# Kernel optimization log

Measured on AMD Instinct MI355X. Metric: run time of the kernel, lower is better.

The kernel has to match this reference:

```python
import math
import jax, jax.numpy as jnp
import numpy as np

B, L, S, H, E, D = 4, 2048, 2048, 8, 64, 64

def setup_inputs() -> dict:
    key = jax.random.key(0)
    kq, kk, kv = jax.random.split(key, 3)
    return {
        "queries": jax.random.normal(kq, (B, L, H, E), dtype=jnp.float32),
        "keys": jax.random.normal(kk, (B, S, H, E), dtype=jnp.float32),
        "values": jax.random.normal(kv, (B, S, H, D), dtype=jnp.float32),
    }

def reference(queries, keys, values):
    E_ = queries.shape[-1]
    scale = 1.0 / math.sqrt(E_)
    # scores: [B, H, L, S]
    scores = jnp.einsum('blhe,bshe->bhls', queries, keys)
    A = jax.nn.softmax(scale * scores, axis=-1)
    # dropout omitted (eval mode / p=0.0)
    out = jnp.einsum('bhls,bshd->blhd', A, values)
    return out
```

## Files before the change

kernel.cpp:

```cpp
#include <hip/hip_runtime.h>
#include <hip/hip_bf16.h>


#define BNUM 4
#define LLEN 2048
#define SLEN 2048
#define HNUM 8
#define EDIM 64

typedef __attribute__((ext_vector_type(8))) short s16x8;
typedef __attribute__((ext_vector_type(8))) _Float16 hf16x8;
typedef __attribute__((ext_vector_type(2))) __fp16 fp16x2;
typedef __attribute__((ext_vector_type(4))) float f32x4;

__device__ __forceinline__ short f2h(float f) {
    union { _Float16 h; short s; } u;
    u.h = (_Float16)f;
    return u.s;
}

__device__ __forceinline__ s16x8 pk8(float4 a, float4 b) {
    union { fp16x2 h[4]; s16x8 v; } u;
    u.h[0] = __builtin_amdgcn_cvt_pkrtz(a.x, a.y);
    u.h[1] = __builtin_amdgcn_cvt_pkrtz(a.z, a.w);
    u.h[2] = __builtin_amdgcn_cvt_pkrtz(b.x, b.y);
    u.h[3] = __builtin_amdgcn_cvt_pkrtz(b.z, b.w);
    return u.v;
}

#if __has_builtin(__builtin_amdgcn_global_load_lds)
#define HAVE_GLL 1
#else
#define HAVE_GLL 0
#endif

__device__ __forceinline__ void stage16(const short* g, short* l) {
#if HAVE_GLL
    __builtin_amdgcn_global_load_lds(
        (const __attribute__((address_space(1))) void*)g,
        (__attribute__((address_space(3))) void*)l, 16, 0, 0);
#else
    *(s16x8*)l = *(const s16x8*)g;
#endif
}

__global__ __launch_bounds__(256)
void prep(const float* __restrict__ Kg, const float* __restrict__ Vg,
          short* __restrict__ Kc, short* __restrict__ Vt)
{
    __shared__ short tile[EDIM][80];
    if (blockIdx.y == 0) {
        const int t = blockIdx.x * 256 + threadIdx.x;
        const int e8 = t & 7;
        const int tmp = t >> 3;
        const int h = tmp & 7;
        const int tmp2 = tmp >> 3;
        const int s = tmp2 & (SLEN - 1);
        const int b = tmp2 >> 11;
        const float4* src = (const float4*)(Kg + (((size_t)(b * SLEN + s) * HNUM + h) * EDIM + e8 * 8));
        float4 a = src[0], bb = src[1];
        *(s16x8*)(Kc + ((size_t)((b * HNUM + h) * SLEN + s) * EDIM + e8 * 8)) = pk8(a, bb);
    } else {
        if (blockIdx.x >= 1024) return;
        const int x = blockIdx.x;
        const int s0 = (x & 31) * 64;
        const int bh = x >> 5;
        const int b = bh >> 3, h = bh & 7;
        {
            const int sr = threadIdx.x >> 2, dc = (threadIdx.x & 3) * 16;
            const float4* src = (const float4*)(Vg + (((size_t)(b * SLEN + s0 + sr) * HNUM + h) * EDIM + dc));
            #pragma unroll
            for (int j4 = 0; j4 < 4; ++j4) {
                float4 a = src[j4];
                tile[dc + j4*4 + 0][sr] = f2h(a.x);
                tile[dc + j4*4 + 1][sr] = f2h(a.y);
                tile[dc + j4*4 + 2][sr] = f2h(a.z);
                tile[dc + j4*4 + 3][sr] = f2h(a.w);
            }
        }
        __syncthreads();
        {
            const int dr = threadIdx.x >> 2, sc = (threadIdx.x & 3) * 16;
            short* dst = Vt + ((size_t)((b * HNUM + h) * EDIM + dr) * SLEN + s0 + sc);
            *(s16x8*)dst       = *(const s16x8*)&tile[dr][sc];
            *(s16x8*)(dst + 8) = *(const s16x8*)&tile[dr][sc + 8];
        }
    }
}

__global__ __launch_bounds__(128, 2)
void fa_fwd(const float* __restrict__ Qg, const short* __restrict__ Kc,
            const short* __restrict__ Vt, float* __restrict__ Og)
{
    __shared__ short sKV[8704];
    __shared__ float sL[2][64];

    const int tid  = threadIdx.x;
    const int wave = tid >> 6;
    const int lane = tid & 63;
    const int m    = lane & 15;
    const int quad = lane >> 4;

    const int lin  = (int)blockIdx.x;
    const int logi = ((lin & 7) << 7) + (lin >> 3);
    const int qx = logi & 31;
    const int h  = (logi >> 5) & 7;
    const int b  = logi >> 8;
    const int qbase = qx * 64;
    const int bh = b * HNUM + h;

    const short* Kbh = Kc + (size_t)bh * SLEN * EDIM;
    const short* Vbh = Vt + (size_t)bh * EDIM * SLEN;

    const int l3 = lane >> 3;
    const int ksrcE = (wave * 32 + l3) * EDIM + ((lane & 7) ^ (l3 & 3)) * 8;
    const int ksrcO = (wave * 32 + l3) * EDIM + ((lane & 7) ^ (4 + (l3 & 3))) * 8;
    const int vsrcB = (lane >> 2) * SLEN + wave * 32 + ((lane & 3) ^ ((lane >> 2) & 3)) * 8;
    short* kdstB = sKV + (wave * 256 + lane) * 8;
    short* vdstB = sKV + 4096 + (wave * 256 + lane) * 8;

#define STAGE_TILE(s0)                                                        \
    do {                                                                      \
        _Pragma("unroll")                                                     \
        for (int p = 0; p < 4; ++p) {                                         \
            const int ks = ((p & 1) ? ksrcO : ksrcE) + (p >> 1) * 1024 + (p & 1) * 512; \
            stage16(Kbh + (size_t)(s0) * EDIM + ks, kdstB + p * 512);         \
            stage16(Vbh + (s0) + vsrcB + p * 16 * SLEN, vdstB + p * 512);     \
        }                                                                     \
    } while (0)

    const float csc = 0.18033688011112042f;
    hf16x8 qfrag[4][2];
    #pragma unroll
    for (int qt = 0; qt < 4; ++qt)
        #pragma unroll
        for (int kb = 0; kb < 2; ++kb) {
            const float* qp = Qg + ((size_t)(b * LLEN + qbase + qt * 16 + m) * HNUM + h) * EDIM
                              + kb * 32 + quad * 8;
            float4 x0 = *(const float4*)qp;
            float4 x1 = *(const float4*)(qp + 4);
            float4 y0 = {x0.x*csc, x0.y*csc, x0.z*csc, x0.w*csc};
            float4 y1 = {x1.x*csc, x1.y*csc, x1.z*csc, x1.w*csc};
            union { s16x8 s; hf16x8 h; } u;
            u.s = pk8(y0, y1);
            qfrag[qt][kb] = u.h;
        }

    const int gk  = ((m >> 2) & 1) * 4 + (m & 3);
    const int pi0 = 8 * (m >> 2) + (m & 3);
    const int kOff00 = (wave * 32 + pi0)     * 64 + ((quad)     ^ gk) * 8;
    const int kOff01 = (wave * 32 + pi0)     * 64 + ((4 + quad) ^ gk) * 8;
    const int kOff10 = (wave * 32 + pi0 + 4) * 64 + ((quad)     ^ gk) * 8;
    const int kOff11 = (wave * 32 + pi0 + 4) * 64 + ((4 + quad) ^ gk) * 8;
    const int vOffB  = 4096 + wave * 2048 + m * 32 + ((quad ^ (m & 3)) * 8);

    hf16x8 vones;
    #pragma unroll
    for (int j = 0; j < 8; ++j) vones[j] = (_Float16)1.0f;

    f32x4 oacc[4][4];
    f32x4 lacc[4];
    #pragma unroll
    for (int i = 0; i < 4; ++i) {
        #pragma unroll
        for (int j = 0; j < 4; ++j) oacc[i][j] = (f32x4){0.f, 0.f, 0.f, 0.f};
        lacc[i] = (f32x4){0.f, 0.f, 0.f, 0.f};
    }

    STAGE_TILE(0);
    __syncthreads();

    for (int s0 = 0; s0 < SLEN; s0 += 64) {
        hf16x8 kf00 = *(const hf16x8*)(sKV + kOff00);
        hf16x8 kf01 = *(const hf16x8*)(sKV + kOff01);
        hf16x8 kf10 = *(const hf16x8*)(sKV + kOff10);
        hf16x8 kf11 = *(const hf16x8*)(sKV + kOff11);
        hf16x8 vf0 = *(const hf16x8*)(sKV + vOffB);
        hf16x8 vf1 = *(const hf16x8*)(sKV + vOffB + 512);
        hf16x8 vf2 = *(const hf16x8*)(sKV + vOffB + 1024);
        hf16x8 vf3 = *(const hf16x8*)(sKV + vOffB + 1536);

        __syncthreads();

        if (s0 + 64 < SLEN) STAGE_TILE(s0 + 64);

        #pragma unroll
        for (int qt = 0; qt < 4; ++qt) {
            f32x4 a0 = {0.f, 0.f, 0.f, 0.f};
            f32x4 a1 = {0.f, 0.f, 0.f, 0.f};
            a0 = __builtin_amdgcn_mfma_f32_16x16x32_f16(kf00, qfrag[qt][0], a0, 0, 0, 0);
            a0 = __builtin_amdgcn_mfma_f32_16x16x32_f16(kf01, qfrag[qt][1], a0, 0, 0, 0);
            a1 = __builtin_amdgcn_mfma_f32_16x16x32_f16(kf10, qfrag[qt][0], a1, 0, 0, 0);
            a1 = __builtin_amdgcn_mfma_f32_16x16x32_f16(kf11, qfrag[qt][1], a1, 0, 0, 0);
            float p0 = __builtin_amdgcn_exp2f(a0[0]);
            float p1 = __builtin_amdgcn_exp2f(a0[1]);
            float p2 = __builtin_amdgcn_exp2f(a0[2]);
            float p3 = __builtin_amdgcn_exp2f(a0[3]);
            float p4 = __builtin_amdgcn_exp2f(a1[0]);
            float p5 = __builtin_amdgcn_exp2f(a1[1]);
            float p6 = __builtin_amdgcn_exp2f(a1[2]);
            float p7 = __builtin_amdgcn_exp2f(a1[3]);
            union { fp16x2 h2[4]; hf16x8 v; } pu;
            pu.h2[0] = __builtin_amdgcn_cvt_pkrtz(p0, p1);
            pu.h2[1] = __builtin_amdgcn_cvt_pkrtz(p2, p3);
            pu.h2[2] = __builtin_amdgcn_cvt_pkrtz(p4, p5);
            pu.h2[3] = __builtin_amdgcn_cvt_pkrtz(p6, p7);
            hf16x8 pf = pu.v;
            lacc[qt] = __builtin_amdgcn_mfma_f32_16x16x32_f16(pf, vones, lacc[qt], 0, 0, 0);
            oacc[qt][0] = __builtin_amdgcn_mfma_f32_16x16x32_f16(pf, vf0, oacc[qt][0], 0, 0, 0);
            oacc[qt][1] = __builtin_amdgcn_mfma_f32_16x16x32_f16(pf, vf1, oacc[qt][1], 0, 0, 0);
            oacc[qt][2] = __builtin_amdgcn_mfma_f32_16x16x32_f16(pf, vf2, oacc[qt][2], 0, 0, 0);
            oacc[qt][3] = __builtin_amdgcn_mfma_f32_16x16x32_f16(pf, vf3, oacc[qt][3], 0, 0, 0);
        }

        __syncthreads();
    }

    if (m == 0) {
        #pragma unroll
        for (int qt = 0; qt < 4; ++qt)
            #pragma unroll
            for (int r = 0; r < 4; ++r)
                sL[wave][qt * 16 + quad * 4 + r] = lacc[qt][r];
    }
    __syncthreads();

    float* sO = (float*)sKV;
    if (wave == 0) {
        #pragma unroll
        for (int qt = 0; qt < 4; ++qt)
            #pragma unroll
            for (int dt = 0; dt < 4; ++dt)
                #pragma unroll
                for (int r = 0; r < 4; ++r)
                    sO[(qt * 16 + quad * 4 + r) * 68 + dt * 16 + m] = oacc[qt][dt][r];
    }
    __syncthreads();
    if (wave == 1) {
        #pragma unroll
        for (int qt = 0; qt < 4; ++qt)
            #pragma unroll
            for (int dt = 0; dt < 4; ++dt)
                #pragma unroll
                for (int r = 0; r < 4; ++r)
                    sO[(qt * 16 + quad * 4 + r) * 68 + dt * 16 + m] += oacc[qt][dt][r];
    }
    __syncthreads();

    {
        const int q = tid >> 1;
        const int dcol = (tid & 1) * 32;
        const float l = sL[0][q] + sL[1][q];
        const float inv = 1.0f / l;
        float* orow = Og + ((size_t)(b * LLEN + qbase + q) * HNUM + h) * EDIM + dcol;
        #pragma unroll
        for (int j = 0; j < 8; ++j) {
            float4 v = *(const float4*)(sO + q * 68 + dcol + j * 4);
            v.x *= inv; v.y *= inv; v.z *= inv; v.w *= inv;
            *(float4*)(orow + j * 4) = v;
        }
    }
}

extern "C" void kernel_launch(void* const* d_in, const int* in_sizes, int n_in,
                              void* d_out, int out_size, void* d_ws, size_t ws_size,
                              hipStream_t stream) {
    const float* Q = (const float*)d_in[0];
    const float* K = (const float*)d_in[1];
    const float* V = (const float*)d_in[2];
    float* O = (float*)d_out;

    const size_t NE = (size_t)BNUM * LLEN * HNUM * EDIM;
    short* Kc = (short*)d_ws;
    short* Vt = Kc + NE;

    prep<<<dim3(2048, 2), dim3(256), 0, stream>>>(K, V, Kc, Vt);
    fa_fwd<<<dim3(1024), dim3(128), 0, stream>>>(Q, Kc, Vt, O);
}
```

Measured before the change: 137.2 us.

## Split keys across four waves per block with 32-query tiles

Reworks the attention kernel to use 256-thread blocks of four waves. Each block now owns 32 queries instead of 64, and each wave processes a 32-key slice of a 128-key staged tile. The grid doubles to 2048 blocks and the per-wave accumulators shrink, so more waves can be resident and the memory latency is spread more finely. In exchange, each block reuses the staged K/V data for half as many queries, and the final cross-wave reduction becomes a serial four-step shared-memory accumulate with a barrier after each step.

```diff
diff --git a/kernel.cpp b/kernel.cpp
--- a/kernel.cpp
+++ b/kernel.cpp
@@ -88,12 +88,12 @@
     }
 }
 
-__global__ __launch_bounds__(128, 2)
+__global__ __launch_bounds__(256, 4)
 void fa_fwd(const float* __restrict__ Qg, const short* __restrict__ Kc,
             const short* __restrict__ Vt, float* __restrict__ Og)
 {
-    __shared__ short sKV[8704];
-    __shared__ float sL[2][64];
+    __shared__ short sKV[16384];
+    __shared__ float sL[4][32];
 
     const int tid  = threadIdx.x;
     const int wave = tid >> 6;
@@ -102,11 +102,11 @@
     const int quad = lane >> 4;
 
     const int lin  = (int)blockIdx.x;
-    const int logi = ((lin & 7) << 7) + (lin >> 3);
-    const int qx = logi & 31;
-    const int h  = (logi >> 5) & 7;
-    const int b  = logi >> 8;
-    const int qbase = qx * 64;
+    const int logi = ((lin & 7) << 8) + (lin >> 3);
+    const int qx = logi & 63;
+    const int h  = (logi >> 6) & 7;
+    const int b  = logi >> 9;
+    const int qbase = qx * 32;
     const int bh = b * HNUM + h;
 
     const short* Kbh = Kc + (size_t)bh * SLEN * EDIM;
@@ -117,7 +117,7 @@
     const int ksrcO = (wave * 32 + l3) * EDIM + ((lane & 7) ^ (4 + (l3 & 3))) * 8;
     const int vsrcB = (lane >> 2) * SLEN + wave * 32 + ((lane & 3) ^ ((lane >> 2) & 3)) * 8;
     short* kdstB = sKV + (wave * 256 + lane) * 8;
-    short* vdstB = sKV + 4096 + (wave * 256 + lane) * 8;
+    short* vdstB = sKV + 8192 + (wave * 256 + lane) * 8;
 
 #define STAGE_TILE(s0)                                                        \
     do {                                                                      \
@@ -130,9 +130,9 @@
     } while (0)
 
     const float csc = 0.18033688011112042f;
-    hf16x8 qfrag[4][2];
-    #pragma unroll
-    for (int qt = 0; qt < 4; ++qt)
+    hf16x8 qfrag[2][2];
+    #pragma unroll
+    for (int qt = 0; qt < 2; ++qt)
         #pragma unroll
         for (int kb = 0; kb < 2; ++kb) {
             const float* qp = Qg + ((size_t)(b * LLEN + qbase + qt * 16 + m) * HNUM + h) * EDIM
@@ -152,16 +152,16 @@
     const int kOff01 = (wave * 32 + pi0)     * 64 + ((4 + quad) ^ gk) * 8;
     const int kOff10 = (wave * 32 + pi0 + 4) * 64 + ((quad)     ^ gk) * 8;
     const int kOff11 = (wave * 32 + pi0 + 4) * 64 + ((4 + quad) ^ gk) * 8;
-    const int vOffB  = 4096 + wave * 2048 + m * 32 + ((quad ^ (m & 3)) * 8);
+    const int vOffB  = 8192 + wave * 2048 + m * 32 + ((quad ^ (m & 3)) * 8);
 
     hf16x8 vones;
     #pragma unroll
     for (int j = 0; j < 8; ++j) vones[j] = (_Float16)1.0f;
 
-    f32x4 oacc[4][4];
-    f32x4 lacc[4];
-    #pragma unroll
-    for (int i = 0; i < 4; ++i) {
+    f32x4 oacc[2][4];
+    f32x4 lacc[2];
+    #pragma unroll
+    for (int i = 0; i < 2; ++i) {
         #pragma unroll
         for (int j = 0; j < 4; ++j) oacc[i][j] = (f32x4){0.f, 0.f, 0.f, 0.f};
         lacc[i] = (f32x4){0.f, 0.f, 0.f, 0.f};
@@ -170,7 +170,7 @@
     STAGE_TILE(0);
     __syncthreads();
 
-    for (int s0 = 0; s0 < SLEN; s0 += 64) {
+    for (int s0 = 0; s0 < SLEN; s0 += 128) {
         hf16x8 kf00 = *(const hf16x8*)(sKV + kOff00);
         hf16x8 kf01 = *(const hf16x8*)(sKV + kOff01);
         hf16x8 kf10 = *(const hf16x8*)(sKV + kOff10);
@@ -182,10 +182,10 @@
 
         __syncthreads();
 
-        if (s0 + 64 < SLEN) STAGE_TILE(s0 + 64);
-
-        #pragma unroll
-        for (int qt = 0; qt < 4; ++qt) {
+        if (s0 + 128 < SLEN) STAGE_TILE(s0 + 128);
+
+        #pragma unroll
+        for (int qt = 0; qt < 2; ++qt) {
             f32x4 a0 = {0.f, 0.f, 0.f, 0.f};
             f32x4 a1 = {0.f, 0.f, 0.f, 0.f};
             a0 = __builtin_amdgcn_mfma_f32_16x16x32_f16(kf00, qfrag[qt][0], a0, 0, 0, 0);
@@ -218,7 +218,7 @@
 
     if (m == 0) {
         #pragma unroll
-        for (int qt = 0; qt < 4; ++qt)
+        for (int qt = 0; qt < 2; ++qt)
             #pragma unroll
             for (int r = 0; r < 4; ++r)
                 sL[wave][qt * 16 + quad * 4 + r] = lacc[qt][r];
@@ -226,39 +226,35 @@
     __syncthreads();
 
     float* sO = (float*)sKV;
-    if (wave == 0) {
-        #pragma unroll
-        for (int qt = 0; qt < 4; ++qt)
+    #pragma unroll
+    for (int w = 0; w < 4; ++w) {
+        if (wave == w) {
             #pragma unroll
-            for (int dt = 0; dt < 4; ++dt)
+            for (int qt = 0; qt < 2; ++qt)
                 #pragma unroll
-                for (int r = 0; r < 4; ++r)
-                    sO[(qt * 16 + quad * 4 + r) * 68 + dt * 16 + m] = oacc[qt][dt][r];
-    }
-    __syncthreads();
-    if (wave == 1) {
-        #pragma unroll
-        for (int qt = 0; qt < 4; ++qt)
-            #pragma unroll
-            for (int dt = 0; dt < 4; ++dt)
-                #pragma unroll
-                for (int r = 0; r < 4; ++r)
-                    sO[(qt * 16 + quad * 4 + r) * 68 + dt * 16 + m] += oacc[qt][dt][r];
-    }
-    __syncthreads();
+                for (int dt = 0; dt < 4; ++dt)
+                    #pragma unroll
+                    for (int r = 0; r < 4; ++r) {
+                        const int idx = (qt * 16 + quad * 4 + r) * 68 + dt * 16 + m;
+                        if (w == 0) sO[idx] = oacc[qt][dt][r];
+                        else        sO[idx] += oacc[qt][dt][r];
+                    }
+        }
+        __syncthreads();
+    }
 
     {
-        const int q = tid >> 1;
-        const int dcol = (tid & 1) * 32;
-        const float l = sL[0][q] + sL[1][q];
+        const int q = tid >> 3;
+        const int dcol = (tid & 7) * 8;
+        const float l = (sL[0][q] + sL[1][q]) + (sL[2][q] + sL[3][q]);
         const float inv = 1.0f / l;
         float* orow = Og + ((size_t)(b * LLEN + qbase + q) * HNUM + h) * EDIM + dcol;
-        #pragma unroll
-        for (int j = 0; j < 8; ++j) {
-            float4 v = *(const float4*)(sO + q * 68 + dcol + j * 4);
-            v.x *= inv; v.y *= inv; v.z *= inv; v.w *= inv;
-            *(float4*)(orow + j * 4) = v;
-        }
+        float4 v0 = *(const float4*)(sO + q * 68 + dcol);
+        float4 v1 = *(const float4*)(sO + q * 68 + dcol + 4);
+        v0.x *= inv; v0.y *= inv; v0.z *= inv; v0.w *= inv;
+        v1.x *= inv; v1.y *= inv; v1.z *= inv; v1.w *= inv;
+        *(float4*)(orow)     = v0;
+        *(float4*)(orow + 4) = v1;
     }
 }
 
@@ -275,5 +271,5 @@
     short* Vt = Kc + NE;
 
     prep<<<dim3(2048, 2), dim3(256), 0, stream>>>(K, V, Kc, Vt);
-    fa_fwd<<<dim3(1024), dim3(128), 0, stream>>>(Q, Kc, Vt, O);
-}
+    fa_fwd<<<dim3(2048), dim3(256), 0, stream>>>(Q, Kc, Vt, O);
+}
```

New measurement: 148.3 us. 1.08x slower.

## Double-buffer K/V LDS staging with prefetch two tiles ahead

Applied to the files above, without the earlier changes.

Doubles the shared K/V buffer so that tile t+2 is loaded asynchronously while tile t is consumed. Fine-grained vmcnt waits and raw s_barrier replace the full __syncthreads around each tile, and the first two tiles are issued before Q is loaded. This is meant to hide global-to-LDS latency behind the MFMA and exp work. In exchange LDS use nearly doubles, which may cut occupancy, and the hand-written waitcnt counts must match the number of stage instructions issued per tile.

```diff
diff --git a/kernel.cpp b/kernel.cpp
--- a/kernel.cpp
+++ b/kernel.cpp
@@ -92,7 +92,7 @@
 void fa_fwd(const float* __restrict__ Qg, const short* __restrict__ Kc,
             const short* __restrict__ Vt, float* __restrict__ Og)
 {
-    __shared__ short sKV[8704];
+    __shared__ short sKV[16384];
     __shared__ float sL[2][64];
 
     const int tid  = threadIdx.x;
@@ -119,15 +119,22 @@
     short* kdstB = sKV + (wave * 256 + lane) * 8;
     short* vdstB = sKV + 4096 + (wave * 256 + lane) * 8;
 
-#define STAGE_TILE(s0)                                                        \
+#define STAGE_TILE(buf, s0)                                                   \
     do {                                                                      \
+        short* kd = kdstB + (buf) * 8192;                                     \
+        short* vd = vdstB + (buf) * 8192;                                     \
         _Pragma("unroll")                                                     \
         for (int p = 0; p < 4; ++p) {                                         \
             const int ks = ((p & 1) ? ksrcO : ksrcE) + (p >> 1) * 1024 + (p & 1) * 512; \
-            stage16(Kbh + (size_t)(s0) * EDIM + ks, kdstB + p * 512);         \
-            stage16(Vbh + (s0) + vsrcB + p * 16 * SLEN, vdstB + p * 512);     \
+            stage16(Kbh + (size_t)(s0) * EDIM + ks, kd + p * 512);            \
+            stage16(Vbh + (s0) + vsrcB + p * 16 * SLEN, vd + p * 512);        \
         }                                                                     \
     } while (0)
+
+    STAGE_TILE(0, 0);
+    asm volatile("" ::: "memory");
+    STAGE_TILE(1, 64);
+    asm volatile("" ::: "memory");
 
     const float csc = 0.18033688011112042f;
     hf16x8 qfrag[4][2];
@@ -141,9 +148,9 @@
             float4 x1 = *(const float4*)(qp + 4);
             float4 y0 = {x0.x*csc, x0.y*csc, x0.z*csc, x0.w*csc};
             float4 y1 = {x1.x*csc, x1.y*csc, x1.z*csc, x1.w*csc};
-            union { s16x8 s; hf16x8 h; } u;
+            union { s16x8 s; hf16x8 hh; } u;
             u.s = pk8(y0, y1);
-            qfrag[qt][kb] = u.h;
+            qfrag[qt][kb] = u.hh;
         }
 
     const int gk  = ((m >> 2) & 1) * 4 + (m & 3);
@@ -167,22 +174,28 @@
         lacc[i] = (f32x4){0.f, 0.f, 0.f, 0.f};
     }
 
-    STAGE_TILE(0);
-    __syncthreads();
-
     for (int s0 = 0; s0 < SLEN; s0 += 64) {
-        hf16x8 kf00 = *(const hf16x8*)(sKV + kOff00);
-        hf16x8 kf01 = *(const hf16x8*)(sKV + kOff01);
-        hf16x8 kf10 = *(const hf16x8*)(sKV + kOff10);
-        hf16x8 kf11 = *(const hf16x8*)(sKV + kOff11);
-        hf16x8 vf0 = *(const hf16x8*)(sKV + vOffB);
-        hf16x8 vf1 = *(const hf16x8*)(sKV + vOffB + 512);
-        hf16x8 vf2 = *(const hf16x8*)(sKV + vOffB + 1024);
-        hf16x8 vf3 = *(const hf16x8*)(sKV + vOffB + 1536);
-
-        __syncthreads();
-
-        if (s0 + 64 < SLEN) STAGE_TILE(s0 + 64);
+        const int t = s0 >> 6;
+        const int bufo = (t & 1) * 8192;
+
+        if (t < SLEN / 64 - 1) asm volatile("s_waitcnt vmcnt(8)" ::: "memory");
+        else                   asm volatile("s_waitcnt vmcnt(0)" ::: "memory");
+        __builtin_amdgcn_s_barrier();
+
+        hf16x8 kf00 = *(const hf16x8*)(sKV + bufo + kOff00);
+        hf16x8 kf01 = *(const hf16x8*)(sKV + bufo + kOff01);
+        hf16x8 kf10 = *(const hf16x8*)(sKV + bufo + kOff10);
+        hf16x8 kf11 = *(const hf16x8*)(sKV + bufo + kOff11);
+        hf16x8 vf0 = *(const hf16x8*)(sKV + bufo + vOffB);
+        hf16x8 vf1 = *(const hf16x8*)(sKV + bufo + vOffB + 512);
+        hf16x8 vf2 = *(const hf16x8*)(sKV + bufo + vOffB + 1024);
+        hf16x8 vf3 = *(const hf16x8*)(sKV + bufo + vOffB + 1536);
+
+        asm volatile("s_waitcnt lgkmcnt(0)" ::: "memory");
+        __builtin_amdgcn_sched_barrier(0);
+        __builtin_amdgcn_s_barrier();
+
+        if (t + 2 < SLEN / 64) STAGE_TILE(t & 1, s0 + 128);
 
         #pragma unroll
         for (int qt = 0; qt < 4; ++qt) {
@@ -212,8 +225,6 @@
             oacc[qt][2] = __builtin_amdgcn_mfma_f32_16x16x32_f16(pf, vf2, oacc[qt][2], 0, 0, 0);
             oacc[qt][3] = __builtin_amdgcn_mfma_f32_16x16x32_f16(pf, vf3, oacc[qt][3], 0, 0, 0);
         }
-
-        __syncthreads();
     }
 
     if (m == 0) {
```

After: 137.2 us. About the same (+0.0%).

## Load K/V fragments directly from global memory into registers with double buffering

Applied to the files above, without the earlier changes.

Removes LDS staging of K and V tiles (global_load_lds plus barriers). Each wave now reads its MFMA fragments straight from global memory into registers, using a two-set ping-pong prefetch so the next tile loads while the current one is computed. This drops the per-tile __syncthreads and LDS traffic. In exchange it uses more registers, and every load is now an uncoalesced 16-byte global read that depends on L2 and L1 caching.

```diff
diff --git a/kernel.cpp b/kernel.cpp
--- a/kernel.cpp
+++ b/kernel.cpp
@@ -26,22 +26,6 @@
     u.h[2] = __builtin_amdgcn_cvt_pkrtz(b.x, b.y);
     u.h[3] = __builtin_amdgcn_cvt_pkrtz(b.z, b.w);
     return u.v;
-}
-
-#if __has_builtin(__builtin_amdgcn_global_load_lds)
-#define HAVE_GLL 1
-#else
-#define HAVE_GLL 0
-#endif
-
-__device__ __forceinline__ void stage16(const short* g, short* l) {
-#if HAVE_GLL
-    __builtin_amdgcn_global_load_lds(
-        (const __attribute__((address_space(1))) void*)g,
-        (__attribute__((address_space(3))) void*)l, 16, 0, 0);
-#else
-    *(s16x8*)l = *(const s16x8*)g;
-#endif
 }
 
 __global__ __launch_bounds__(256)
@@ -92,7 +76,7 @@
 void fa_fwd(const float* __restrict__ Qg, const short* __restrict__ Kc,
             const short* __restrict__ Vt, float* __restrict__ Og)
 {
-    __shared__ short sKV[8704];
+    __shared__ float sO[64 * 68];
     __shared__ float sL[2][64];
 
     const int tid  = threadIdx.x;
@@ -112,23 +96,6 @@
     const short* Kbh = Kc + (size_t)bh * SLEN * EDIM;
     const short* Vbh = Vt + (size_t)bh * EDIM * SLEN;
 
-    const int l3 = lane >> 3;
-    const int ksrcE = (wave * 32 + l3) * EDIM + ((lane & 7) ^ (l3 & 3)) * 8;
-    const int ksrcO = (wave * 32 + l3) * EDIM + ((lane & 7) ^ (4 + (l3 & 3))) * 8;
-    const int vsrcB = (lane >> 2) * SLEN + wave * 32 + ((lane & 3) ^ ((lane >> 2) & 3)) * 8;
-    short* kdstB = sKV + (wave * 256 + lane) * 8;
-    short* vdstB = sKV + 4096 + (wave * 256 + lane) * 8;
-
-#define STAGE_TILE(s0)                                                        \
-    do {                                                                      \
-        _Pragma("unroll")                                                     \
-        for (int p = 0; p < 4; ++p) {                                         \
-            const int ks = ((p & 1) ? ksrcO : ksrcE) + (p >> 1) * 1024 + (p & 1) * 512; \
-            stage16(Kbh + (size_t)(s0) * EDIM + ks, kdstB + p * 512);         \
-            stage16(Vbh + (s0) + vsrcB + p * 16 * SLEN, vdstB + p * 512);     \
-        }                                                                     \
-    } while (0)
-
     const float csc = 0.18033688011112042f;
     hf16x8 qfrag[4][2];
     #pragma unroll
@@ -141,18 +108,14 @@
             float4 x1 = *(const float4*)(qp + 4);
             float4 y0 = {x0.x*csc, x0.y*csc, x0.z*csc, x0.w*csc};
             float4 y1 = {x1.x*csc, x1.y*csc, x1.z*csc, x1.w*csc};
-            union { s16x8 s; hf16x8 h; } u;
+            union { s16x8 s; hf16x8 hh; } u;
             u.s = pk8(y0, y1);
-            qfrag[qt][kb] = u.h;
-        }
-
-    const int gk  = ((m >> 2) & 1) * 4 + (m & 3);
+            qfrag[qt][kb] = u.hh;
+        }
+
     const int pi0 = 8 * (m >> 2) + (m & 3);
-    const int kOff00 = (wave * 32 + pi0)     * 64 + ((quad)     ^ gk) * 8;
-    const int kOff01 = (wave * 32 + pi0)     * 64 + ((4 + quad) ^ gk) * 8;
-    const int kOff10 = (wave * 32 + pi0 + 4) * 64 + ((quad)     ^ gk) * 8;
-    const int kOff11 = (wave * 32 + pi0 + 4) * 64 + ((4 + quad) ^ gk) * 8;
-    const int vOffB  = 4096 + wave * 2048 + m * 32 + ((quad ^ (m & 3)) * 8);
+    const short* kbase = Kbh + (wave * 32 + pi0) * EDIM + quad * 8;
+    const short* vbase = Vbh + (size_t)m * SLEN + wave * 32 + quad * 8;
 
     hf16x8 vones;
     #pragma unroll
@@ -167,53 +130,64 @@
         lacc[i] = (f32x4){0.f, 0.f, 0.f, 0.f};
     }
 
-    STAGE_TILE(0);
-    __syncthreads();
-
-    for (int s0 = 0; s0 < SLEN; s0 += 64) {
-        hf16x8 kf00 = *(const hf16x8*)(sKV + kOff00);
-        hf16x8 kf01 = *(const hf16x8*)(sKV + kOff01);
-        hf16x8 kf10 = *(const hf16x8*)(sKV + kOff10);
-        hf16x8 kf11 = *(const hf16x8*)(sKV + kOff11);
-        hf16x8 vf0 = *(const hf16x8*)(sKV + vOffB);
-        hf16x8 vf1 = *(const hf16x8*)(sKV + vOffB + 512);
-        hf16x8 vf2 = *(const hf16x8*)(sKV + vOffB + 1024);
-        hf16x8 vf3 = *(const hf16x8*)(sKV + vOffB + 1536);
-
-        __syncthreads();
-
-        if (s0 + 64 < SLEN) STAGE_TILE(s0 + 64);
-
-        #pragma unroll
-        for (int qt = 0; qt < 4; ++qt) {
-            f32x4 a0 = {0.f, 0.f, 0.f, 0.f};
-            f32x4 a1 = {0.f, 0.f, 0.f, 0.f};
-            a0 = __builtin_amdgcn_mfma_f32_16x16x32_f16(kf00, qfrag[qt][0], a0, 0, 0, 0);
-            a0 = __builtin_amdgcn_mfma_f32_16x16x32_f16(kf01, qfrag[qt][1], a0, 0, 0, 0);
-            a1 = __builtin_amdgcn_mfma_f32_16x16x32_f16(kf10, qfrag[qt][0], a1, 0, 0, 0);
-            a1 = __builtin_amdgcn_mfma_f32_16x16x32_f16(kf11, qfrag[qt][1], a1, 0, 0, 0);
-            float p0 = __builtin_amdgcn_exp2f(a0[0]);
-            float p1 = __builtin_amdgcn_exp2f(a0[1]);
-            float p2 = __builtin_amdgcn_exp2f(a0[2]);
-            float p3 = __builtin_amdgcn_exp2f(a0[3]);
-            float p4 = __builtin_amdgcn_exp2f(a1[0]);
-            float p5 = __builtin_amdgcn_exp2f(a1[1]);
-            float p6 = __builtin_amdgcn_exp2f(a1[2]);
-            float p7 = __builtin_amdgcn_exp2f(a1[3]);
-            union { fp16x2 h2[4]; hf16x8 v; } pu;
-            pu.h2[0] = __builtin_amdgcn_cvt_pkrtz(p0, p1);
-            pu.h2[1] = __builtin_amdgcn_cvt_pkrtz(p2, p3);
-            pu.h2[2] = __builtin_amdgcn_cvt_pkrtz(p4, p5);
-            pu.h2[3] = __builtin_amdgcn_cvt_pkrtz(p6, p7);
-            hf16x8 pf = pu.v;
-            lacc[qt] = __builtin_amdgcn_mfma_f32_16x16x32_f16(pf, vones, lacc[qt], 0, 0, 0);
-            oacc[qt][0] = __builtin_amdgcn_mfma_f32_16x16x32_f16(pf, vf0, oacc[qt][0], 0, 0, 0);
-            oacc[qt][1] = __builtin_amdgcn_mfma_f32_16x16x32_f16(pf, vf1, oacc[qt][1], 0, 0, 0);
-            oacc[qt][2] = __builtin_amdgcn_mfma_f32_16x16x32_f16(pf, vf2, oacc[qt][2], 0, 0, 0);
-            oacc[qt][3] = __builtin_amdgcn_mfma_f32_16x16x32_f16(pf, vf3, oacc[qt][3], 0, 0, 0);
-        }
-
-        __syncthreads();
+    hf16x8 kA00, kA01, kA10, kA11, vA0, vA1, vA2, vA3;
+    hf16x8 kB00, kB01, kB10, kB11, vB0, vB1, vB2, vB3;
+
+#define LOADF(K00, K01, K10, K11, V0, V1, V2, V3, S0)                         \
+    do {                                                                      \
+        const short* kp = kbase + (size_t)(S0) * EDIM;                        \
+        const short* vp = vbase + (S0);                                       \
+        K00 = *(const hf16x8*)(kp);                                           \
+        K01 = *(const hf16x8*)(kp + 32);                                      \
+        K10 = *(const hf16x8*)(kp + 4 * EDIM);                                \
+        K11 = *(const hf16x8*)(kp + 4 * EDIM + 32);                           \
+        V0  = *(const hf16x8*)(vp);                                           \
+        V1  = *(const hf16x8*)(vp + 16 * SLEN);                               \
+        V2  = *(const hf16x8*)(vp + 32 * SLEN);                               \
+        V3  = *(const hf16x8*)(vp + 48 * SLEN);                               \
+    } while (0)
+
+#define COMPUTE(K00, K01, K10, K11, V0, V1, V2, V3)                           \
+    do {                                                                      \
+        _Pragma("unroll")                                                     \
+        for (int qt = 0; qt < 4; ++qt) {                                      \
+            f32x4 a0 = {0.f, 0.f, 0.f, 0.f};                                  \
+            f32x4 a1 = {0.f, 0.f, 0.f, 0.f};                                  \
+            a0 = __builtin_amdgcn_mfma_f32_16x16x32_f16(K00, qfrag[qt][0], a0, 0, 0, 0); \
+            a0 = __builtin_amdgcn_mfma_f32_16x16x32_f16(K01, qfrag[qt][1], a0, 0, 0, 0); \
+            a1 = __builtin_amdgcn_mfma_f32_16x16x32_f16(K10, qfrag[qt][0], a1, 0, 0, 0); \
+            a1 = __builtin_amdgcn_mfma_f32_16x16x32_f16(K11, qfrag[qt][1], a1, 0, 0, 0); \
+            float p0 = __builtin_amdgcn_exp2f(a0[0]);                         \
+            float p1 = __builtin_amdgcn_exp2f(a0[1]);                         \
+            float p2 = __builtin_amdgcn_exp2f(a0[2]);                         \
+            float p3 = __builtin_amdgcn_exp2f(a0[3]);                         \
+            float p4 = __builtin_amdgcn_exp2f(a1[0]);                         \
+            float p5 = __builtin_amdgcn_exp2f(a1[1]);                         \
+            float p6 = __builtin_amdgcn_exp2f(a1[2]);                         \
+            float p7 = __builtin_amdgcn_exp2f(a1[3]);                         \
+            union { fp16x2 h2[4]; hf16x8 v; } pu;                             \
+            pu.h2[0] = __builtin_amdgcn_cvt_pkrtz(p0, p1);                    \
+            pu.h2[1] = __builtin_amdgcn_cvt_pkrtz(p2, p3);                    \
+            pu.h2[2] = __builtin_amdgcn_cvt_pkrtz(p4, p5);                    \
+            pu.h2[3] = __builtin_amdgcn_cvt_pkrtz(p6, p7);                    \
+            hf16x8 pf = pu.v;                                                 \
+            lacc[qt] = __builtin_amdgcn_mfma_f32_16x16x32_f16(pf, vones, lacc[qt], 0, 0, 0); \
+            oacc[qt][0] = __builtin_amdgcn_mfma_f32_16x16x32_f16(pf, V0, oacc[qt][0], 0, 0, 0); \
+            oacc[qt][1] = __builtin_amdgcn_mfma_f32_16x16x32_f16(pf, V1, oacc[qt][1], 0, 0, 0); \
+            oacc[qt][2] = __builtin_amdgcn_mfma_f32_16x16x32_f16(pf, V2, oacc[qt][2], 0, 0, 0); \
+            oacc[qt][3] = __builtin_amdgcn_mfma_f32_16x16x32_f16(pf, V3, oacc[qt][3], 0, 0, 0); \
+        }                                                                     \
+    } while (0)
+
+    LOADF(kA00, kA01, kA10, kA11, vA0, vA1, vA2, vA3, 0);
+
+    for (int t = 0; t < 32; t += 2) {
+        const int s1 = (t + 1) * 64;
+        LOADF(kB00, kB01, kB10, kB11, vB0, vB1, vB2, vB3, s1);
+        COMPUTE(kA00, kA01, kA10, kA11, vA0, vA1, vA2, vA3);
+        const int s2 = (t + 2 < 32) ? (t + 2) * 64 : s1;
+        LOADF(kA00, kA01, kA10, kA11, vA0, vA1, vA2, vA3, s2);
+        COMPUTE(kB00, kB01, kB10, kB11, vB0, vB1, vB2, vB3);
     }
 
     if (m == 0) {
@@ -225,7 +199,6 @@
     }
     __syncthreads();
 
-    float* sO = (float*)sKV;
     if (wave == 0) {
         #pragma unroll
         for (int qt = 0; qt < 4; ++qt)
```

Result: slower. 159.6 us (+16.3%).
